# Optimization experiments

Hardware: AMD Instinct MI355X
Metric: run time of the kernel (lower is better)

The kernel has to match this reference:

```python
import jax, jax.numpy as jnp
import numpy as np

N_TAPERS = 3  # standard edgetaper iteration count used in vdeblur

def psf2otf(psf, shape):
    # zero-pad psf to `shape` and circularly shift so kernel center -> (0,0), then FFT
    kh, kw = psf.shape[-2], psf.shape[-1]
    pad = [(0, 0)] * (psf.ndim - 2) + [(0, shape[0] - kh), (0, shape[1] - kw)]
    p = jnp.pad(psf, pad)
    p = jnp.roll(p, shift=(-(kh // 2), -(kw // 2)), axis=(-2, -1))
    return jnp.fft.fft2(p)

def edgetaper_alpha(kernel, shape):
    # kernel: [kh,kw]; builds the separable taper window from kernel autocorrelation
    vs = []
    for i in range(2):
        proj = jnp.sum(kernel, axis=1 - i)
        z = jnp.fft.fft(proj, shape[i] - 1)
        z = jnp.fft.ifft(jnp.abs(z) ** 2).real
        z = jnp.concatenate([z, z[:1]])
        vs.append(1.0 - z / jnp.max(z))
    return jnp.outer(vs[0], vs[1])

def edgetaper_one(img, kernel):
    # img: [C,Hp,Wp], kernel: [kh,kw]; blend image with its circular blur near borders
    shape = img.shape[-2:]
    alpha = edgetaper_alpha(kernel, shape)[None]          # [1,Hp,Wp]
    otf = psf2otf(kernel, shape)[None]                    # [1,Hp,Wp] complex
    for _ in range(N_TAPERS):
        blurred = jnp.fft.ifft2(jnp.fft.fft2(img) * otf).real
        img = alpha * img + (1.0 - alpha) * blurred
    return img

def setup_inputs() -> dict:
    key = jax.random.key(0)
    k1, k2, k3, k4 = jax.random.split(key, 4)
    B, C, H, W = 8, 3, 512, 512
    KH = KW = 31
    NF, FS = 8, 3
    y = jax.random.uniform(k1, (B, C, H, W), dtype=jnp.float32)
    k = jax.random.uniform(k2, (B, 1, KH, KW), dtype=jnp.float32)
    k = k / jnp.sum(k, axis=(-2, -1), keepdims=True)       # normalized blur PSF
    lam = jax.random.uniform(k3, (), dtype=jnp.float32)    # nn.Parameter(torch.rand(1).squeeze())
    fan_in = C * FS * FS
    filters = jax.random.normal(k4, (NF, C, FS, FS), dtype=jnp.float32) * np.sqrt(2.0 / fan_in)
    return {"y": y, "k": k, "lam": lam, "filters": filters}

def reference(y, k, lam, filters):
    kh, kw = k.shape[-2], k.shape[-1]
    ph, pw = (kh - 1) // 2, (kw - 1) // 2
    # pad_for_kernel (edge replicate) + edgetaper
    x = jnp.pad(y, ((0, 0), (0, 0), (ph, ph), (pw, pw)), mode='edge')
    x = jax.vmap(edgetaper_one)(x, k[:, 0])
    H, W = x.shape[-2], x.shape[-1]
    Fy = jnp.fft.fft2(x)                                   # [B,C,H,W] complex (== rfft onesided=False)
    Dg = psf2otf(filters, (H, W))                          # [NF,C,H,W]
    Dk = psf2otf(k, (H, W))                                # [B,1,H,W], broadcasts over C
    exp_lam = jnp.exp(lam)
    Dg_sum = jnp.sum(jnp.abs(Dg) ** 2, axis=0)[None] * exp_lam   # [1,C,H,W]
    Omega = 1.0 / (jnp.abs(Dk) ** 2 + Dg_sum)              # [B,C,H,W]
    out = jnp.fft.ifft2(Omega * jnp.conj(Dk) * Fy).real    # irfft onesided=False
    return out
```

## Files before the change

### kernel.cpp

```cpp
#include <hip/hip_runtime.h>
#include <cmath>

#define HH 542
#define KH 271
#define NPIX (HH*HH)
#define BB 8
#define CC3 3
#define NCH (BB*CC3)
#define NP 12
#define MROWS (NP*HH)
#define KSZ 31
#define KRAD 15
#define NF 8
#define FS 3

#define NSPLIT 2
#define NGRP 40
#define BTSZ (NGRP*NSPLIT*17*512)

typedef __attribute__((ext_vector_type(8))) short short8v;
typedef __attribute__((ext_vector_type(4))) float float4v;

static __device__ __forceinline__ float2 cmul(float2 a, float2 b) {
    return make_float2(a.x*b.x - a.y*b.y, a.x*b.y + a.y*b.x);
}

static __device__ __forceinline__ void pair_chans(int p, int& n1, int& n2) {
    if (p < 8) { n1 = 3*p;     n2 = 3*p + 1; }
    else       { int q = p-8; n1 = 6*q + 2; n2 = 6*q + 5; }
}

static __device__ __forceinline__ void split2_pack_pair(float x, float y,
        unsigned& p0, unsigned& p1) {
    unsigned ux = __float_as_uint(x), uy = __float_as_uint(y);
    unsigned hx0 = (ux + 0x8000u) & 0xffff0000u;
    unsigned hy0 = (uy + 0x8000u) & 0xffff0000u;
    float rx = x - __uint_as_float(hx0);
    float ry = y - __uint_as_float(hy0);
    unsigned hx1 = (__float_as_uint(rx) + 0x8000u) & 0xffff0000u;
    unsigned hy1 = (__float_as_uint(ry) + 0x8000u) & 0xffff0000u;
    p0 = (hx0 >> 16) | hy0;
    p1 = (hx1 >> 16) | hy1;
}

__global__ void gen_tables(float2* tw542, short* Btf, short* Bti) {
    int idx = blockIdx.x*blockDim.x + threadIdx.x;
    const float PI2 = 6.283185307179586f;
    if (idx < HH) {
        float ang = -PI2*(float)idx/(float)HH;
        float s, c; sincosf(ang, &s, &c);
        tw542[idx] = make_float2(c, s);
    }
    if (idx >= BTSZ) return;
    int j    = idx & 7;
    int lane = (idx >> 3) & 63;
    int rem  = idx >> 9;
    int step = rem % 17;
    int rem2 = rem / 17;
    int s    = rem2 % NSPLIT;
    int g    = rem2 / NSPLIT;
    if (g >= NGRP) return;
    int o  = (g >= 20) ? 1 : 0;
    int v1 = (g - 20*o)*16 + (lane & 15);
    int kq = step*32 + (lane >> 4)*8 + j;
    int kidx = kq >> 1, c = kq & 1;
    float wre = 0.f, wim = 0.f;
    if (v1 < KH && kidx < KH) {
        int r = (kidx*v1) % KH;
        float ang = -PI2*(float)r/(float)KH;
        float sn, cs; sincosf(ang, &sn, &cs);
        wre = cs; wim = sn;
    }
    float vf = (o==0) ? ((c==0) ? wre : -wim) : ((c==0) ?  wim : wre);
    float vi = (o==0) ? ((c==0) ? wre :  wim) : ((c==0) ? -wim : wre);
    {
        unsigned u = __float_as_uint(vf);
        unsigned h0 = (u + 0x8000u) & 0xffff0000u;
        float r1 = vf - __uint_as_float(h0);
        unsigned h1 = (__float_as_uint(r1) + 0x8000u) & 0xffff0000u;
        Btf[idx] = (short)(((s==0) ? h0 : h1) >> 16);
    }
    {
        unsigned u = __float_as_uint(vi);
        unsigned h0 = (u + 0x8000u) & 0xffff0000u;
        float r1 = vi - __uint_as_float(h0);
        unsigned h1 = (__float_as_uint(r1) + 0x8000u) & 0xffff0000u;
        Bti[idx] = (short)(((s==0) ? h0 : h1) >> 16);
    }
}

__global__ void alpha_kernel(const float* __restrict__ kk, float* __restrict__ valpha) {
    int b = blockIdx.x;
    int t = threadIdx.x;
    __shared__ float proj[2][KSZ];
    __shared__ float ac[2][KSZ];
    const float* kb = kk + b*KSZ*KSZ;
    if (t < KSZ) {
        float s = 0;
        for (int j = 0; j < KSZ; j++) s += kb[t*KSZ + j];
        proj[0][t] = s;
    } else if (t >= 32 && t < 32+KSZ) {
        int j = t - 32;
        float s = 0;
        for (int i = 0; i < KSZ; i++) s += kb[i*KSZ + j];
        proj[1][j] = s;
    }
    __syncthreads();
    if (t < KSZ) {
        float s0 = 0, s1 = 0;
        for (int m = 0; m + t < KSZ; m++) {
            s0 += proj[0][m]*proj[0][m+t];
            s1 += proj[1][m]*proj[1][m+t];
        }
        ac[0][t] = s0; ac[1][t] = s1;
    }
    __syncthreads();
    float inv0 = 1.0f/ac[0][0];
    float inv1 = 1.0f/ac[1][0];
    for (int d = t; d < HH; d += blockDim.x) {
        for (int a = 0; a < 2; a++) {
            float z;
            if (d <= 30)                   z = ac[a][d];
            else if (d >= 511 && d <= 540) z = ac[a][541-d];
            else if (d == 541)             z = ac[a][0];
            else                           z = 0.0f;
            valpha[(b*2 + a)*HH + d] = 1.0f - z*(a ? inv1 : inv0);
        }
    }
}

__global__ void dk_stage1(const float* __restrict__ kk, const float2* __restrict__ tw,
                          float2* __restrict__ T1) {
    int idx = blockIdx.x*blockDim.x + threadIdx.x;
    if (idx >= BB*KSZ*HH) return;
    int v  = idx % HH;
    int bm = idx / HH;
    int m  = bm % KSZ;
    int b  = bm / KSZ;
    const float* kb = kk + (b*KSZ + m)*KSZ;
    float2 w  = tw[(KRAD*(HH - v)) % HH];
    float2 ru = tw[v];
    float2 acc = make_float2(0.f, 0.f);
    for (int n = 0; n < KSZ; n++) {
        float kv = kb[n];
        acc.x = fmaf(kv, w.x, acc.x);
        acc.y = fmaf(kv, w.y, acc.y);
        float wx = w.x*ru.x - w.y*ru.y;
        float wy = w.x*ru.y + w.y*ru.x;
        w = make_float2(wx, wy);
    }
    T1[idx] = acc;
}

#define UT2 8
__global__ void dk_stage2(const float2* __restrict__ T1, const float2* __restrict__ tw,
                          float2* __restrict__ Dk) {
    int bid = blockIdx.x;
    int vc = bid % 3;
    int rem = bid / 3;
    int ut = rem % 68;
    int b  = rem / 68;
    int v = vc*256 + threadIdx.x;
    if (v >= HH) return;
    int u0 = ut*UT2;
    float2 acc[UT2], w[UT2], ru[UT2];
    #pragma unroll
    for (int uu = 0; uu < UT2; uu++) {
        int u = u0 + uu;
        int uc = (u < HH) ? u : 0;
        acc[uu] = make_float2(0.f, 0.f);
        w[uu]  = tw[(KRAD*(HH - uc)) % HH];
        ru[uu] = tw[uc];
    }
    const float2* t1 = T1 + (size_t)b*KSZ*HH + v;
    for (int m = 0; m < KSZ; m++) {
        float2 t = t1[(size_t)m*HH];
        #pragma unroll
        for (int uu = 0; uu < UT2; uu++) {
            acc[uu].x = fmaf(t.x, w[uu].x, fmaf(-t.y, w[uu].y, acc[uu].x));
            acc[uu].y = fmaf(t.x, w[uu].y, fmaf( t.y, w[uu].x, acc[uu].y));
            float wx = w[uu].x*ru[uu].x - w[uu].y*ru[uu].y;
            float wy = w[uu].x*ru[uu].y + w[uu].y*ru[uu].x;
            w[uu] = make_float2(wx, wy);
        }
    }
    #pragma unroll
    for (int uu = 0; uu < UT2; uu++) {
        int u = u0 + uu;
        if (u < HH) Dk[(size_t)b*NPIX + (size_t)u*HH + v] = acc[uu];
    }
}

__global__ void dgs_kernel(const float* __restrict__ filt, const float* __restrict__ lamp,
                           const float2* __restrict__ tw, float* __restrict__ Dgs) {
    int uv = blockIdx.x*blockDim.x + threadIdx.x;
    if (uv >= NPIX) return;
    int u = uv / HH;
    int v = uv - u*HH;
    float el = expf(lamp[0]);
    float2 wu[3], wv[3];
    wu[0] = tw[u ? HH-u : 0]; wu[1] = make_float2(1.f,0.f); wu[2] = tw[u];
    wv[0] = tw[v ? HH-v : 0]; wv[1] = make_float2(1.f,0.f); wv[2] = tw[v];
    float2 ph[3][3];
    #pragma unroll
    for (int m = 0; m < 3; m++)
        #pragma unroll
        for (int n = 0; n < 3; n++)
            ph[m][n] = cmul(wu[m], wv[n]);
    for (int c = 0; c < CC3; c++) {
        float s = 0.f;
        for (int f = 0; f < NF; f++) {
            float2 acc = make_float2(0.f, 0.f);
            const float* fp = filt + ((f*CC3 + c)*FS)*FS;
            #pragma unroll
            for (int m = 0; m < 3; m++)
                #pragma unroll
                for (int n = 0; n < 3; n++) {
                    float fv = fp[m*3+n];
                    acc.x = fmaf(fv, ph[m][n].x, acc.x);
                    acc.y = fmaf(fv, ph[m][n].y, acc.y);
                }
            s = fmaf(acc.x, acc.x, fmaf(acc.y, acc.y, s));
        }
        Dgs[c*NPIX + uv] = s*el;
    }
}

__global__ void pad_pack(const float* __restrict__ y, float* __restrict__ R0,
                         float2* __restrict__ CA) {
    int idx = blockIdx.x*blockDim.x + threadIdx.x;
    if (idx >= NP*NPIX) return;
    int uv = idx % NPIX;
    int p  = idx / NPIX;
    int n1, n2; pair_chans(p, n1, n2);
    int i = uv / HH, j = uv - i*HH;
    int yi = min(max(i - KRAD, 0), 511);
    int yj = min(max(j - KRAD, 0), 511);
    int yo = yi*512 + yj;
    float v1 = y[(size_t)n1*262144 + yo];
    float v2 = y[(size_t)n2*262144 + yo];
    R0[(size_t)n1*NPIX + uv] = v1;
    R0[(size_t)n2*NPIX + uv] = v2;
    CA[idx] = make_float2(v1, v2);
}

__global__ void specmul(const float2* __restrict__ CA, const float2* __restrict__ Dk,
                        const float* __restrict__ Dgs, float2* __restrict__ CB, int mode) {
    int idx = blockIdx.x*blockDim.x + threadIdx.x;
    if (idx >= NP*NPIX) return;
    int uv = idx % NPIX;
    int p  = idx / NPIX;
    int n1, n2; pair_chans(p, n1, n2);
    int b1 = n1/3, c1 = n1 - 3*b1;
    int b2 = n2/3, c2 = n2 - 3*b2;
    int i = uv / HH, j = uv - i*HH;
    int ni = i ? HH - i : 0;
    int nj = j ? HH - j : 0;
    float2 Z  = CA[(size_t)p*NPIX + uv];
    float2 Zm = CA[(size_t)p*NPIX + ni*HH + nj];
    float2 F1 = make_float2(0.5f*(Z.x + Zm.x), 0.5f*(Z.y - Zm.y));
    float2 F2 = make_float2(0.5f*(Z.y + Zm.y), 0.5f*(Zm.x - Z.x));
    float2 d1 = Dk[(size_t)b1*NPIX + uv];
    float2 d2 = Dk[(size_t)b2*NPIX + uv];
    float2 M1, M2;
    if (mode == 0) {
        M1 = d1; M2 = d2;
    } else {
        float o1 = 1.0f/(d1.x*d1.x + d1.y*d1.y + Dgs[(size_t)c1*NPIX + uv]);
        float o2 = 1.0f/(d2.x*d2.x + d2.y*d2.y + Dgs[(size_t)c2*NPIX + uv]);
        M1 = make_float2(d1.x*o1, -d1.y*o1);
        M2 = make_float2(d2.x*o2, -d2.y*o2);
    }
    float2 W1 = cmul(M1, F1);
    float2 W2 = cmul(M2, F2);
    CB[idx] = make_float2(W1.x - W2.y, W1.y + W2.x);
}

__global__ void __launch_bounds__(256, 4)
fft_mfma(const float2* __restrict__ Ain, float2* __restrict__ Aout,
         const short* __restrict__ Bt, const float2* __restrict__ tw542,
         const float* __restrict__ valp, float* __restrict__ R0,
         float* __restrict__ outbuf, float scale, int conjtw, int mode)
{
    __shared__ char smem[17408];
    short* As = (short*)smem;
    float4* Tsf = (float4*)smem;
    const int APL = 64*40;

    int id = blockIdx.x;
    int xcd = id & 7, jj = id >> 3;
    int lin = xcd*128 + jj;
    if (lin >= 1020) return;
    int by = lin / 5, bx = lin - 5*by;

    int tid = threadIdx.x;
    int arow = tid >> 3, ai4 = tid & 7;
    int wid = tid >> 6, lane = tid & 63;
    int l15 = lane & 15, quad = lane >> 4;

    int aoff0 = l15*40 + quad*8;

    const short* pB[2];
    #pragma unroll
    for (int ct = 0; ct < 2; ct++) {
        int grp = (ct ? 20 : 0) + bx*4 + wid;
        pB[ct] = Bt + (size_t)grp*(NSPLIT*17*512) + lane*8;
    }

    float4v acc[4][2];
    #pragma unroll
    for (int mt = 0; mt < 4; mt++)
        #pragma unroll
        for (int ct = 0; ct < 2; ct++)
            acc[mt][ct] = (float4v)(0.f);

    float4 regA[2][2];
    short8v bf[2][2][2];
    const float4 z4 = make_float4(0.f,0.f,0.f,0.f);

    int rowg = by*32 + arow;
    bool rvld = rowg < MROWS;
    const float4* rp = (const float4*)Ain + (size_t)(rvld ? rowg : 0)*271;

    auto loadA = [&](int buf, int step) {
        int i0 = step*16 + 2*ai4;
        regA[buf][0] = (rvld && i0     < 271) ? rp[i0]   : z4;
        regA[buf][1] = (rvld && i0 + 1 < 271) ? rp[i0+1] : z4;
    };
    auto loadB = [&](int buf, int step) {
        #pragma unroll
        for (int ct = 0; ct < 2; ct++)
            #pragma unroll
            for (int s = 0; s < NSPLIT; s++)
                bf[buf][ct][s] = *(const short8v*)(pB[ct] + ((s*17 + step) << 9));
    };

    loadA(0, 0); loadB(0, 0);

    #pragma unroll 2
    for (int step = 0; step < 17; step++) {
        int cur = step & 1, nxt = cur ^ 1;
        {
            int rl = 2*arow;
            int offE = rl*40 + 4*ai4;
            float4 f0 = regA[cur][0], f1 = regA[cur][1];
            unsigned e0a,e1a, e0b,e1b;
            split2_pack_pair(f0.x, f0.y, e0a, e1a);
            split2_pack_pair(f1.x, f1.y, e0b, e1b);
            *(uint2*)(As + 0*APL + offE) = make_uint2(e0a, e0b);
            *(uint2*)(As + 1*APL + offE) = make_uint2(e1a, e1b);
            unsigned o0a,o1a, o0b,o1b;
            split2_pack_pair(f0.z, f0.w, o0a, o1a);
            split2_pack_pair(f1.z, f1.w, o0b, o1b);
            int offO = offE + 40;
            *(uint2*)(As + 0*APL + offO) = make_uint2(o0a, o0b);
            *(uint2*)(As + 1*APL + offO) = make_uint2(o1a, o1b);
        }
        __syncthreads();

        if (step + 1 < 17) { loadA(nxt, step+1); loadB(nxt, step+1); }

        #pragma unroll
        for (int sa = 0; sa < 2; sa++) {
            short8v af[4];
            #pragma unroll
            for (int mt = 0; mt < 4; mt++)
                af[mt] = *(const short8v*)(As + sa*APL + aoff0 + mt*16*40);
            #pragma unroll
            for (int sb = 0; sb + sa < 2; sb++)
                #pragma unroll
                for (int mt = 0; mt < 4; mt++)
                    #pragma unroll
                    for (int ct = 0; ct < 2; ct++)
                        acc[mt][ct] = __builtin_amdgcn_mfma_f32_16x16x32_bf16(
                            af[mt], bf[cur][ct][sb], acc[mt][ct], 0, 0, 0);
        }
        __syncthreads();
    }

    float2 tg;
    {
        int v1g = (bx*4 + wid)*16 + l15;
        tg = tw542[(v1g < HH) ? v1g : 0];
        if (conjtw) tg.y = -tg.y;
    }

    int lane16 = tid & 15;
    int rrow = tid >> 4;
    int r0 = by*32 + 2*lane16;
    bool rok = r0 < MROWS;
    int plane = rok ? (r0 / HH) : 0;
    int colg = r0 - plane*HH;
    int n1, n2; pair_chans(plane, n1, n2);
    int b1 = n1/3, b2 = n2/3;

    #pragma unroll
    for (int half = 0; half < 2; half++) {
        __syncthreads();
        #pragma unroll
        for (int mt = 0; mt < 4; mt++) {
            float2 v[2];
            #pragma unroll
            for (int pr = 0; pr < 2; pr++) {
                float Ere = acc[mt][0][2*pr], Ore = acc[mt][0][2*pr+1];
                float Eim = acc[mt][1][2*pr], Oim = acc[mt][1][2*pr+1];
                float tOre = tg.x*Ore - tg.y*Oim;
                float tOim = tg.x*Oim + tg.y*Ore;
                v[pr] = (half == 0)
                    ? make_float2((Ere + tOre)*scale, (Eim + tOim)*scale)
                    : make_float2((Ere - tOre)*scale, (Eim - tOim)*scale);
            }
            int v1loc = wid*16 + l15;
            int uu = mt*4 + quad;
            Tsf[v1loc*17 + uu] = make_float4(v[0].x, v[0].y, v[1].x, v[1].y);
        }
        __syncthreads();
        #pragma unroll
        for (int it = 0; it < 4; it++) {
            int v1loc = rrow + it*16;
            int v1g2 = bx*64 + v1loc;
            if (v1g2 >= KH || !rok) continue;
            int v1 = v1g2 + (half ? KH : 0);
            float4 f = Tsf[v1loc*17 + lane16];
            size_t sp = (size_t)v1*HH + colg;
            if (mode == 0) {
                *(float4*)(Aout + (size_t)plane*NPIX + sp) = f;
            } else if (mode == 1) {
                float ar1 = valp[b1*2*HH + v1];
                float ar2 = valp[b2*2*HH + v1];
                float ac1a = valp[(b1*2+1)*HH + colg];
                float ac1b = valp[(b1*2+1)*HH + colg + 1];
                float ac2a = valp[(b2*2+1)*HH + colg];
                float ac2b = valp[(b2*2+1)*HH + colg + 1];
                float2* p1 = (float2*)(R0 + (size_t)n1*NPIX + sp);
                float2* p2 = (float2*)(R0 + (size_t)n2*NPIX + sp);
                float2 o1 = *p1, o2 = *p2;
                float nv1a = fmaf(ar1*ac1a, o1.x - f.x, f.x);
                float nv1b = fmaf(ar1*ac1b, o1.y - f.z, f.z);
                float nv2a = fmaf(ar2*ac2a, o2.x - f.y, f.y);
                float nv2b = fmaf(ar2*ac2b, o2.y - f.w, f.w);
                *p1 = make_float2(nv1a, nv1b);
                *p2 = make_float2(nv2a, nv2b);
                *(float4*)(Aout + (size_t)plane*NPIX + sp) =
                    make_float4(nv1a, nv2a, nv1b, nv2b);
            } else {
                *(float2*)(outbuf + (size_t)n1*NPIX + sp) = make_float2(f.x, f.z);
                *(float2*)(outbuf + (size_t)n2*NPIX + sp) = make_float2(f.y, f.w);
            }
        }
    }
}

extern "C" void kernel_launch(void* const* d_in, const int* in_sizes, int n_in,
                              void* d_out, int out_size, void* d_ws, size_t ws_size,
                              hipStream_t stream) {
    const float* y    = (const float*)d_in[0];
    const float* k    = (const float*)d_in[1];
    const float* lam  = (const float*)d_in[2];
    const float* filt = (const float*)d_in[3];
    float* out = (float*)d_out;

    char* base = (char*)d_ws;
    size_t off = 0;
    auto alloc = [&](size_t bytes) {
        void* p = base + off;
        off = (off + bytes + 511) & ~(size_t)511;
        return p;
    };
    float2* CA   = (float2*)alloc(sizeof(float2)*(size_t)NP*NPIX);
    float2* CB   = (float2*)alloc(sizeof(float2)*(size_t)NP*NPIX);
    float*  R0   = (float*) alloc(sizeof(float)*(size_t)NCH*NPIX);
    float2* Dk   = (float2*)alloc(sizeof(float2)*(size_t)BB*NPIX);
    float2* T1   = (float2*)alloc(sizeof(float2)*(size_t)BB*KSZ*HH);
    float*  Dgs  = (float*) alloc(sizeof(float)*(size_t)CC3*NPIX);
    short*  Btf  = (short*) alloc(sizeof(short)*(size_t)BTSZ);
    short*  Bti  = (short*) alloc(sizeof(short)*(size_t)BTSZ);
    float2* tw   = (float2*)alloc(sizeof(float2)*(size_t)HH);
    float*  valp = (float*) alloc(sizeof(float)*(size_t)BB*2*HH);
    (void)ws_size; (void)in_sizes; (void)n_in; (void)out_size;

    const int TPB = 256;
    auto nb = [](long n) { return (int)((n + 255)/256); };

    gen_tables<<<nb((long)BTSZ), TPB, 0, stream>>>(tw, Btf, Bti);
    alpha_kernel<<<BB, 64, 0, stream>>>(k, valp);
    dk_stage1<<<nb((long)BB*KSZ*HH), TPB, 0, stream>>>(k, tw, T1);
    dk_stage2<<<8*68*3, TPB, 0, stream>>>(T1, tw, Dk);
    dgs_kernel<<<nb((long)NPIX), TPB, 0, stream>>>(filt, lam, tw, Dgs);
    pad_pack<<<nb((long)NP*NPIX), TPB, 0, stream>>>(y, R0, CA);

    const int FG = 1024;
    const float isc = 1.0f/(float)HH;
    float2 *S = CA, *T = CB;
    fft_mfma<<<FG, TPB, 0, stream>>>(S, T, Btf, tw, valp, R0, out, 1.0f, 0, 0);
    fft_mfma<<<FG, TPB, 0, stream>>>(T, S, Btf, tw, valp, R0, out, 1.0f, 0, 0);
    for (int it = 0; it < 3; it++) {
        specmul<<<nb((long)NP*NPIX), TPB, 0, stream>>>(S, Dk, Dgs, T, 0);
        fft_mfma<<<FG, TPB, 0, stream>>>(T, S, Bti, tw, valp, R0, out, isc, 1, 0);
        fft_mfma<<<FG, TPB, 0, stream>>>(S, T, Bti, tw, valp, R0, out, isc, 1, 1);
        fft_mfma<<<FG, TPB, 0, stream>>>(T, S, Btf, tw, valp, R0, out, 1.0f, 0, 0);
        fft_mfma<<<FG, TPB, 0, stream>>>(S, T, Btf, tw, valp, R0, out, 1.0f, 0, 0);
        float2* tmp = S; S = T; T = tmp;
    }
    specmul<<<nb((long)NP*NPIX), TPB, 0, stream>>>(S, Dk, Dgs, T, 1);
    fft_mfma<<<FG, TPB, 0, stream>>>(T, S, Bti, tw, valp, R0, out, isc, 1, 0);
    fft_mfma<<<FG, TPB, 0, stream>>>(S, T, Bti, tw, valp, R0, out, isc, 1, 2);
}
```

Measured before the change: 775.7 us.

## Halve FFT-GEMM row tile to 16 rows and raise occupancy target

Each fft_mfma block now handles 16 rows instead of 32. It uses half the LDS, half the accumulators and a single-buffered B fragment, and the block remap and grid size are changed to cover twice as many blocks. The launch bound asks for 8 waves-per-EU-worth of blocks instead of 4, to fit more blocks per CU and hide latency. In exchange, every B fragment is reloaded from global memory for each 16-row tile, which halves B reuse, and the B loads are no longer prefetched one step ahead.

```diff
diff --git a/kernel.cpp b/kernel.cpp
--- a/kernel.cpp
+++ b/kernel.cpp
@@ -276,25 +276,25 @@
     CB[idx] = make_float2(W1.x - W2.y, W1.y + W2.x);
 }
 
-__global__ void __launch_bounds__(256, 4)
+__global__ void __launch_bounds__(256, 8)
 fft_mfma(const float2* __restrict__ Ain, float2* __restrict__ Aout,
          const short* __restrict__ Bt, const float2* __restrict__ tw542,
          const float* __restrict__ valp, float* __restrict__ R0,
          float* __restrict__ outbuf, float scale, int conjtw, int mode)
 {
-    __shared__ char smem[17408];
+    __shared__ char smem[9216];
     short* As = (short*)smem;
     float4* Tsf = (float4*)smem;
-    const int APL = 64*40;
+    const int APL = 32*40;
 
     int id = blockIdx.x;
     int xcd = id & 7, jj = id >> 3;
-    int lin = xcd*128 + jj;
-    if (lin >= 1020) return;
+    int lin = xcd*255 + jj;
+    if (lin >= 2035) return;
     int by = lin / 5, bx = lin - 5*by;
 
     int tid = threadIdx.x;
-    int arow = tid >> 3, ai4 = tid & 7;
+    int arow = tid >> 4, ai8 = tid & 15;
     int wid = tid >> 6, lane = tid & 63;
     int l15 = lane & 15, quad = lane >> 4;
 
@@ -307,73 +307,68 @@
         pB[ct] = Bt + (size_t)grp*(NSPLIT*17*512) + lane*8;
     }
 
-    float4v acc[4][2];
+    float4v acc[2][2];
     #pragma unroll
-    for (int mt = 0; mt < 4; mt++)
+    for (int mt = 0; mt < 2; mt++)
         #pragma unroll
         for (int ct = 0; ct < 2; ct++)
             acc[mt][ct] = (float4v)(0.f);
 
-    float4 regA[2][2];
-    short8v bf[2][2][2];
+    float4 regA[2];
+    short8v bf[2][2];
     const float4 z4 = make_float4(0.f,0.f,0.f,0.f);
 
-    int rowg = by*32 + arow;
+    int rowg = by*16 + arow;
     bool rvld = rowg < MROWS;
     const float4* rp = (const float4*)Ain + (size_t)(rvld ? rowg : 0)*271;
 
     auto loadA = [&](int buf, int step) {
-        int i0 = step*16 + 2*ai4;
-        regA[buf][0] = (rvld && i0     < 271) ? rp[i0]   : z4;
-        regA[buf][1] = (rvld && i0 + 1 < 271) ? rp[i0+1] : z4;
+        int i0 = step*16 + ai8;
+        regA[buf] = (rvld && i0 < 271) ? rp[i0] : z4;
     };
-    auto loadB = [&](int buf, int step) {
+    auto loadB = [&](int step) {
         #pragma unroll
         for (int ct = 0; ct < 2; ct++)
             #pragma unroll
             for (int s = 0; s < NSPLIT; s++)
-                bf[buf][ct][s] = *(const short8v*)(pB[ct] + ((s*17 + step) << 9));
+                bf[ct][s] = *(const short8v*)(pB[ct] + ((s*17 + step) << 9));
     };
 
-    loadA(0, 0); loadB(0, 0);
+    loadA(0, 0);
 
     #pragma unroll 2
     for (int step = 0; step < 17; step++) {
         int cur = step & 1, nxt = cur ^ 1;
+        loadB(step);
         {
-            int rl = 2*arow;
-            int offE = rl*40 + 4*ai4;
-            float4 f0 = regA[cur][0], f1 = regA[cur][1];
-            unsigned e0a,e1a, e0b,e1b;
-            split2_pack_pair(f0.x, f0.y, e0a, e1a);
-            split2_pack_pair(f1.x, f1.y, e0b, e1b);
-            *(uint2*)(As + 0*APL + offE) = make_uint2(e0a, e0b);
-            *(uint2*)(As + 1*APL + offE) = make_uint2(e1a, e1b);
-            unsigned o0a,o1a, o0b,o1b;
-            split2_pack_pair(f0.z, f0.w, o0a, o1a);
-            split2_pack_pair(f1.z, f1.w, o0b, o1b);
-            int offO = offE + 40;
-            *(uint2*)(As + 0*APL + offO) = make_uint2(o0a, o0b);
-            *(uint2*)(As + 1*APL + offO) = make_uint2(o1a, o1b);
+            int off = (2*arow)*40 + 2*ai8;
+            float4 f = regA[cur];
+            unsigned e0, e1, o0, o1;
+            split2_pack_pair(f.x, f.y, e0, e1);
+            split2_pack_pair(f.z, f.w, o0, o1);
+            *(unsigned*)(As + 0*APL + off)      = e0;
+            *(unsigned*)(As + 1*APL + off)      = e1;
+            *(unsigned*)(As + 0*APL + off + 40) = o0;
+            *(unsigned*)(As + 1*APL + off + 40) = o1;
         }
         __syncthreads();
 
-        if (step + 1 < 17) { loadA(nxt, step+1); loadB(nxt, step+1); }
+        if (step + 1 < 17) loadA(nxt, step + 1);
 
         #pragma unroll
         for (int sa = 0; sa < 2; sa++) {
-            short8v af[4];
+            short8v af[2];
             #pragma unroll
-            for (int mt = 0; mt < 4; mt++)
+            for (int mt = 0; mt < 2; mt++)
                 af[mt] = *(const short8v*)(As + sa*APL + aoff0 + mt*16*40);
             #pragma unroll
             for (int sb = 0; sb + sa < 2; sb++)
                 #pragma unroll
-                for (int mt = 0; mt < 4; mt++)
+                for (int mt = 0; mt < 2; mt++)
                     #pragma unroll
                     for (int ct = 0; ct < 2; ct++)
                         acc[mt][ct] = __builtin_amdgcn_mfma_f32_16x16x32_bf16(
-                            af[mt], bf[cur][ct][sb], acc[mt][ct], 0, 0, 0);
+                            af[mt], bf[ct][sb], acc[mt][ct], 0, 0, 0);
         }
         __syncthreads();
     }
@@ -385,9 +380,9 @@
         if (conjtw) tg.y = -tg.y;
     }
 
-    int lane16 = tid & 15;
-    int rrow = tid >> 4;
-    int r0 = by*32 + 2*lane16;
+    int lane8 = tid & 7;
+    int rrow = tid >> 3;
+    int r0 = by*16 + 2*lane8;
     bool rok = r0 < MROWS;
     int plane = rok ? (r0 / HH) : 0;
     int colg = r0 - plane*HH;
@@ -398,7 +393,7 @@
     for (int half = 0; half < 2; half++) {
         __syncthreads();
         #pragma unroll
-        for (int mt = 0; mt < 4; mt++) {
+        for (int mt = 0; mt < 2; mt++) {
             float2 v[2];
             #pragma unroll
             for (int pr = 0; pr < 2; pr++) {
@@ -412,16 +407,16 @@
             }
             int v1loc = wid*16 + l15;
             int uu = mt*4 + quad;
-            Tsf[v1loc*17 + uu] = make_float4(v[0].x, v[0].y, v[1].x, v[1].y);
+            Tsf[v1loc*9 + uu] = make_float4(v[0].x, v[0].y, v[1].x, v[1].y);
         }
         __syncthreads();
         #pragma unroll
-        for (int it = 0; it < 4; it++) {
-            int v1loc = rrow + it*16;
+        for (int it = 0; it < 2; it++) {
+            int v1loc = rrow + it*32;
             int v1g2 = bx*64 + v1loc;
             if (v1g2 >= KH || !rok) continue;
             int v1 = v1g2 + (half ? KH : 0);
-            float4 f = Tsf[v1loc*17 + lane16];
+            float4 f = Tsf[v1loc*9 + lane8];
             size_t sp = (size_t)v1*HH + colg;
             if (mode == 0) {
                 *(float4*)(Aout + (size_t)plane*NPIX + sp) = f;
@@ -489,7 +484,7 @@
     dgs_kernel<<<nb((long)NPIX), TPB, 0, stream>>>(filt, lam, tw, Dgs);
     pad_pack<<<nb((long)NP*NPIX), TPB, 0, stream>>>(y, R0, CA);
 
-    const int FG = 1024;
+    const int FG = 2040;
     const float isc = 1.0f/(float)HH;
     float2 *S = CA, *T = CB;
     fft_mfma<<<FG, TPB, 0, stream>>>(S, T, Btf, tw, valp, R0, out, 1.0f, 0, 0);
```

Result: slower. 1.175 ms (+51.5%).
